# Performance work log

Hardware: AMD Instinct MI355X
Metric: run time of the kernel (lower is better)

Reference implementation:

```python
import jax, jax.numpy as jnp
import numpy as np

INPUT_WINDOW = 2048
HEAD_DIM = 128  # embedding_size // number_of_heads = 2048 // 16
TAU = 1.0
SCALE = 1.0 / ((INPUT_WINDOW * HEAD_DIM) ** 0.5 * TAU)


def setup_inputs() -> dict:
    key = jax.random.key(0)
    # (batch, number_of_series, length_input_window, hidden_dimensionality)
    x = jax.random.normal(key, (8, 16, 2048, 128), dtype=jnp.float32)
    return {"x": x}


def reference(x) -> jnp.ndarray:
    # Q = K = V = x; scores: [B, S, W, W]
    qk = jnp.einsum("bswd,bsud->bswu", x, x) * SCALE
    attn = jax.nn.softmax(qk, axis=-1)
    # dropout(p=0.1) is identity in eval mode
    out = jnp.einsum("bswu,bsud->bswd", attn, x)
    return out
```

## Files before the change

### kernel.cpp

```cpp
#include <hip/hip_runtime.h>
#include <hip/hip_bf16.h>


#define NSEQ   2048
#define DIM    128
#define KVBLK  64
#define EC (1.44269504088896f / 512.0f)

typedef short s8v __attribute__((ext_vector_type(8)));
typedef float f4   __attribute__((ext_vector_type(4)));
typedef float f16v __attribute__((ext_vector_type(16)));
typedef unsigned int u2 __attribute__((ext_vector_type(2)));
typedef unsigned int u4 __attribute__((ext_vector_type(4)));

__device__ __forceinline__ unsigned pk2(float a, float b) {
    union { __hip_bfloat162 h; unsigned u; } c;
    c.h = __float22bfloat162_rn(make_float2(a, b));
    return c.u;
}

__global__ __launch_bounds__(256, 2)
void attn_fwd(const float* __restrict__ x, float* __restrict__ out) {
    const int bid  = blockIdx.x;
    const int wg   = (bid & 7) * 256 + (bid >> 3);
    const int head = wg >> 4;
    const int qb   = wg & 15;

    const float* __restrict__ xh = x   + (size_t)head * (NSEQ * DIM);
    float* __restrict__       oh = out + (size_t)head * (NSEQ * DIM);

    const int tid  = threadIdx.x;
    const int lane = tid & 63;
    const int wave = tid >> 6;
    const int l31  = lane & 31;
    const int h    = lane >> 5;

    __shared__ __align__(16) short sK [KVBLK * DIM];
    __shared__ __align__(16) short sVt[DIM * KVBLK];

    const int qw0 = qb * 128 + wave * 32;
    s8v Qf[8];
    {
        const float* qp = xh + (size_t)(qw0 + l31) * DIM + 8 * h;
#pragma unroll
        for (int ks = 0; ks < 8; ++ks) {
            f4 a = *(const f4*)(qp + ks * 16);
            f4 b = *(const f4*)(qp + ks * 16 + 4);
            u4 q = { pk2(a[0], a[1]), pk2(a[2], a[3]), pk2(b[0], b[1]), pk2(b[2], b[3]) };
            Qf[ks] = *(s8v*)&q;
        }
    }

    f16v accO[4];
#pragma unroll
    for (int dt = 0; dt < 4; ++dt) accO[dt] = (f16v)(0.f);
    float lsum = 0.f;

    const int rw = tid >> 4;
    const int cg = tid & 15;

    f4 ld[8];
    {
        const float* s = xh + (size_t)(4 * rw) * DIM + 8 * cg;
#pragma unroll
        for (int i = 0; i < 4; ++i) {
            ld[2*i]   = *(const f4*)(s + i * DIM);
            ld[2*i+1] = *(const f4*)(s + i * DIM + 4);
        }
    }

    for (int kv0 = 0; kv0 < NSEQ; kv0 += KVBLK) {
#pragma unroll
        for (int i = 0; i < 4; ++i) {
            const int r  = 4 * rw + i;
            const int sz = ((r & 7) ^ ((r >> 3) & 7)) << 3;
            u4 kv = { pk2(ld[2*i][0],   ld[2*i][1]),   pk2(ld[2*i][2],   ld[2*i][3]),
                      pk2(ld[2*i+1][0], ld[2*i+1][1]), pk2(ld[2*i+1][2], ld[2*i+1][3]) };
            *(u4*)&sK[(r * DIM + 8 * cg) ^ sz] = kv;
        }
#pragma unroll
        for (int j = 0; j < 8; ++j) {
            const int d  = 8 * cg + j;
            const int sz = ((d & 7) ^ ((d >> 3) & 7)) << 3;
            const int hi = j >> 2, jj = j & 3;
            u2 vv = { pk2(ld[0 + hi][jj], ld[2 + hi][jj]),
                      pk2(ld[4 + hi][jj], ld[6 + hi][jj]) };
            *(u2*)&sVt[(d * KVBLK + 4 * rw) ^ sz] = vv;
        }
        __syncthreads();

        f16v accS[2];
        accS[0] = (f16v)(0.f); accS[1] = (f16v)(0.f);
        __builtin_amdgcn_s_setprio(1);
#pragma unroll
        for (int ut = 0; ut < 2; ++ut) {
            const int r    = ut * 32 + l31;
            const int sz   = ((r & 7) ^ ((r >> 3) & 7)) << 3;
            const int base = r * DIM + 8 * h;
#pragma unroll
            for (int ks = 0; ks < 8; ++ks) {
                s8v Kf = *(const s8v*)&sK[(base + ks * 16) ^ sz];
                accS[ut] = __builtin_amdgcn_mfma_f32_32x32x16_bf16(
                    Kf, Qf[ks], accS[ut], 0, 0, 0);
            }
        }
        __builtin_amdgcn_s_setprio(0);

        if (kv0 + KVBLK < NSEQ) {
            const float* s = xh + (size_t)(kv0 + KVBLK + 4 * rw) * DIM + 8 * cg;
#pragma unroll
            for (int i = 0; i < 4; ++i) {
                ld[2*i]   = *(const f4*)(s + i * DIM);
                ld[2*i+1] = *(const f4*)(s + i * DIM + 4);
            }
        }

        float part = 0.f;
#pragma unroll
        for (int ut = 0; ut < 2; ++ut)
#pragma unroll
            for (int r = 0; r < 16; ++r) {
                float v = exp2f(accS[ut][r] * EC);
                accS[ut][r] = v;
                part += v;
            }
        lsum += part;

        s8v Pf[4];
#pragma unroll
        for (int ks = 0; ks < 4; ++ks) {
#define PP(f) accS[(f) >> 4][(f) & 15]
            unsigned pa0 = pk2(PP(8*ks + 0), PP(8*ks + 1));
            unsigned pa1 = pk2(PP(8*ks + 2), PP(8*ks + 3));
            unsigned pb0 = pk2(PP(8*ks + 4), PP(8*ks + 5));
            unsigned pb1 = pk2(PP(8*ks + 6), PP(8*ks + 7));
#undef PP
            auto t0 = __builtin_amdgcn_permlane32_swap(pa0, pb0, false, false);
            auto t1 = __builtin_amdgcn_permlane32_swap(pa1, pb1, false, false);
            u4 w = { (unsigned)t0[0], (unsigned)t1[0], (unsigned)t0[1], (unsigned)t1[1] };
            Pf[ks] = *(s8v*)&w;
        }

        __builtin_amdgcn_s_setprio(1);
#pragma unroll
        for (int dt = 0; dt < 4; ++dt) {
            const int d    = dt * 32 + l31;
            const int sz   = ((d & 7) ^ ((d >> 3) & 7)) << 3;
            const int base = d * KVBLK + 8 * h;
#pragma unroll
            for (int ks = 0; ks < 4; ++ks) {
                s8v Vf = *(const s8v*)&sVt[(base + ks * 16) ^ sz];
                accO[dt] = __builtin_amdgcn_mfma_f32_32x32x16_bf16(
                    Pf[ks], Vf, accO[dt], 0, 0, 0);
            }
        }
        __builtin_amdgcn_s_setprio(0);
        __syncthreads();
    }

    const float tot = lsum + __shfl_xor(lsum, 32);
    const float inv = 1.f / tot;
#pragma unroll
    for (int r = 0; r < 16; ++r) {
        const int q       = (r & 3) + 8 * (r >> 2) + 4 * h;
        const float invq  = __shfl(inv, q, 32);
        float* op = oh + (size_t)(qw0 + q) * DIM + l31;
#pragma unroll
        for (int dt = 0; dt < 4; ++dt)
            op[dt * 32] = accO[dt][r] * invq;
    }
}

extern "C" void kernel_launch(void* const* d_in, const int* in_sizes, int n_in,
                              void* d_out, int out_size, void* d_ws, size_t ws_size,
                              hipStream_t stream) {
    const float* x = (const float*)d_in[0];
    float* out     = (float*)d_out;
    hipLaunchKernelGGL(attn_fwd, dim3(2048), dim3(256), 0, stream, x, out);
}
```

Measured before the change: 368.8 us.

## Pre-convert K/V to swizzled bf16 tiles and DMA them into double-buffered LDS

Adds a prepass kernel that converts each head's fp32 input into bf16 K and transposed V tiles already in the swizzled LDS layout, stored in the workspace. The attention kernel then streams these tiles with global_load_lds into double-buffered shared memory, overlapping the next tile's load with compute. This removes the repeated per-workgroup fp32 loads and bf16 conversion. It also folds the softmax scale into Q and uses the raw exp2 builtin. It costs an extra kernel launch, a large workspace with a fallback path, and doubled LDS usage.

```diff
diff --git a/kernel.cpp b/kernel.cpp
--- a/kernel.cpp
+++ b/kernel.cpp
@@ -5,6 +5,8 @@
 #define NSEQ   2048
 #define DIM    128
 #define KVBLK  64
+#define TILES  (NSEQ / KVBLK)
+#define IMG    (KVBLK * DIM)
 #define EC (1.44269504088896f / 512.0f)
 
 typedef short s8v __attribute__((ext_vector_type(8)));
@@ -13,14 +15,53 @@
 typedef unsigned int u2 __attribute__((ext_vector_type(2)));
 typedef unsigned int u4 __attribute__((ext_vector_type(4)));
 
+typedef __attribute__((address_space(1))) const void glob_t;
+typedef __attribute__((address_space(3))) void lds_t;
+
 __device__ __forceinline__ unsigned pk2(float a, float b) {
     union { __hip_bfloat162 h; unsigned u; } c;
     c.h = __float22bfloat162_rn(make_float2(a, b));
     return c.u;
 }
+__device__ __forceinline__ int swz(int r) { return ((r & 7) ^ ((r >> 3) & 7)) << 3; }
+
+__global__ __launch_bounds__(256)
+void prepass(const float* __restrict__ x, short* __restrict__ wsK,
+             short* __restrict__ wsV) {
+    const int b = blockIdx.x;
+    const float* src = x + (size_t)b * IMG;
+    short* dK = wsK + (size_t)b * IMG;
+    short* dV = wsV + (size_t)b * IMG;
+    const int rw = threadIdx.x >> 4;
+    const int cg = threadIdx.x & 15;
+
+    f4 ld[8];
+    const float* s = src + (size_t)(4 * rw) * DIM + 8 * cg;
+#pragma unroll
+    for (int i = 0; i < 4; ++i) {
+        ld[2*i]   = *(const f4*)(s + i * DIM);
+        ld[2*i+1] = *(const f4*)(s + i * DIM + 4);
+    }
+#pragma unroll
+    for (int i = 0; i < 4; ++i) {
+        const int r = 4 * rw + i;
+        u4 kv = { pk2(ld[2*i][0],   ld[2*i][1]),   pk2(ld[2*i][2],   ld[2*i][3]),
+                  pk2(ld[2*i+1][0], ld[2*i+1][1]), pk2(ld[2*i+1][2], ld[2*i+1][3]) };
+        *(u4*)&dK[(r * DIM + 8 * cg) ^ swz(r)] = kv;
+    }
+#pragma unroll
+    for (int j = 0; j < 8; ++j) {
+        const int d  = 8 * cg + j;
+        const int hi = j >> 2, jj = j & 3;
+        u2 vv = { pk2(ld[0 + hi][jj], ld[2 + hi][jj]),
+                  pk2(ld[4 + hi][jj], ld[6 + hi][jj]) };
+        *(u2*)&dV[(d * KVBLK + 4 * rw) ^ swz(d)] = vv;
+    }
+}
 
 __global__ __launch_bounds__(256, 2)
-void attn_fwd(const float* __restrict__ x, float* __restrict__ out) {
+void attn_lds(const float* __restrict__ x, const short* __restrict__ wsK,
+              const short* __restrict__ wsV, float* __restrict__ out) {
     const int bid  = blockIdx.x;
     const int wg   = (bid & 7) * 256 + (bid >> 3);
     const int head = wg >> 4;
@@ -28,6 +69,8 @@
 
     const float* __restrict__ xh = x   + (size_t)head * (NSEQ * DIM);
     float* __restrict__       oh = out + (size_t)head * (NSEQ * DIM);
+    const short* gK = wsK + (size_t)head * TILES * IMG;
+    const short* gV = wsV + (size_t)head * TILES * IMG;
 
     const int tid  = threadIdx.x;
     const int lane = tid & 63;
@@ -35,8 +78,8 @@
     const int l31  = lane & 31;
     const int h    = lane >> 5;
 
-    __shared__ __align__(16) short sK [KVBLK * DIM];
-    __shared__ __align__(16) short sVt[DIM * KVBLK];
+    __shared__ __align__(16) short sK [2][IMG];
+    __shared__ __align__(16) short sVt[2][IMG];
 
     const int qw0 = qb * 128 + wave * 32;
     s8v Qf[8];
@@ -46,7 +89,8 @@
         for (int ks = 0; ks < 8; ++ks) {
             f4 a = *(const f4*)(qp + ks * 16);
             f4 b = *(const f4*)(qp + ks * 16 + 4);
-            u4 q = { pk2(a[0], a[1]), pk2(a[2], a[3]), pk2(b[0], b[1]), pk2(b[2], b[3]) };
+            u4 q = { pk2(a[0] * EC, a[1] * EC), pk2(a[2] * EC, a[3] * EC),
+                     pk2(b[0] * EC, b[1] * EC), pk2(b[2] * EC, b[3] * EC) };
             Qf[ks] = *(s8v*)&q;
         }
     }
@@ -56,38 +100,25 @@
     for (int dt = 0; dt < 4; ++dt) accO[dt] = (f16v)(0.f);
     float lsum = 0.f;
 
-    const int rw = tid >> 4;
-    const int cg = tid & 15;
-
-    f4 ld[8];
-    {
-        const float* s = xh + (size_t)(4 * rw) * DIM + 8 * cg;
+    const int so = wave * 512 + lane * 8;
+    auto stage = [&](int b, int t) {
+        const short* srcK = gK + (size_t)t * IMG + so;
+        const short* srcV = gV + (size_t)t * IMG + so;
 #pragma unroll
         for (int i = 0; i < 4; ++i) {
-            ld[2*i]   = *(const f4*)(s + i * DIM);
-            ld[2*i+1] = *(const f4*)(s + i * DIM + 4);
-        }
-    }
-
-    for (int kv0 = 0; kv0 < NSEQ; kv0 += KVBLK) {
-#pragma unroll
-        for (int i = 0; i < 4; ++i) {
-            const int r  = 4 * rw + i;
-            const int sz = ((r & 7) ^ ((r >> 3) & 7)) << 3;
-            u4 kv = { pk2(ld[2*i][0],   ld[2*i][1]),   pk2(ld[2*i][2],   ld[2*i][3]),
-                      pk2(ld[2*i+1][0], ld[2*i+1][1]), pk2(ld[2*i+1][2], ld[2*i+1][3]) };
-            *(u4*)&sK[(r * DIM + 8 * cg) ^ sz] = kv;
-        }
-#pragma unroll
-        for (int j = 0; j < 8; ++j) {
-            const int d  = 8 * cg + j;
-            const int sz = ((d & 7) ^ ((d >> 3) & 7)) << 3;
-            const int hi = j >> 2, jj = j & 3;
-            u2 vv = { pk2(ld[0 + hi][jj], ld[2 + hi][jj]),
-                      pk2(ld[4 + hi][jj], ld[6 + hi][jj]) };
-            *(u2*)&sVt[(d * KVBLK + 4 * rw) ^ sz] = vv;
-        }
-        __syncthreads();
+            __builtin_amdgcn_global_load_lds((glob_t*)(srcK + i * 2048),
+                (lds_t*)&sK[b][wave * 512 + i * 2048], 16, 0, 0);
+            __builtin_amdgcn_global_load_lds((glob_t*)(srcV + i * 2048),
+                (lds_t*)&sVt[b][wave * 512 + i * 2048], 16, 0, 0);
+        }
+    };
+
+    stage(0, 0);
+    __syncthreads();
+    int buf = 0;
+
+    for (int t = 0; t < TILES; ++t) {
+        if (t + 1 < TILES) stage(buf ^ 1, t + 1);
 
         f16v accS[2];
         accS[0] = (f16v)(0.f); accS[1] = (f16v)(0.f);
@@ -95,32 +126,23 @@
 #pragma unroll
         for (int ut = 0; ut < 2; ++ut) {
             const int r    = ut * 32 + l31;
-            const int sz   = ((r & 7) ^ ((r >> 3) & 7)) << 3;
-            const int base = r * DIM + 8 * h;
+            const int base = (r * DIM + 8 * h);
+            const int sz   = swz(r);
 #pragma unroll
             for (int ks = 0; ks < 8; ++ks) {
-                s8v Kf = *(const s8v*)&sK[(base + ks * 16) ^ sz];
+                s8v Kf = *(const s8v*)&sK[buf][(base + ks * 16) ^ sz];
                 accS[ut] = __builtin_amdgcn_mfma_f32_32x32x16_bf16(
                     Kf, Qf[ks], accS[ut], 0, 0, 0);
             }
         }
         __builtin_amdgcn_s_setprio(0);
 
-        if (kv0 + KVBLK < NSEQ) {
-            const float* s = xh + (size_t)(kv0 + KVBLK + 4 * rw) * DIM + 8 * cg;
-#pragma unroll
-            for (int i = 0; i < 4; ++i) {
-                ld[2*i]   = *(const f4*)(s + i * DIM);
-                ld[2*i+1] = *(const f4*)(s + i * DIM + 4);
-            }
-        }
-
         float part = 0.f;
 #pragma unroll
         for (int ut = 0; ut < 2; ++ut)
 #pragma unroll
             for (int r = 0; r < 16; ++r) {
-                float v = exp2f(accS[ut][r] * EC);
+                float v = __builtin_amdgcn_exp2f(accS[ut][r]);
                 accS[ut][r] = v;
                 part += v;
             }
@@ -145,8 +167,148 @@
 #pragma unroll
         for (int dt = 0; dt < 4; ++dt) {
             const int d    = dt * 32 + l31;
-            const int sz   = ((d & 7) ^ ((d >> 3) & 7)) << 3;
             const int base = d * KVBLK + 8 * h;
+            const int sz   = swz(d);
+#pragma unroll
+            for (int ks = 0; ks < 4; ++ks) {
+                s8v Vf = *(const s8v*)&sVt[buf][(base + ks * 16) ^ sz];
+                accO[dt] = __builtin_amdgcn_mfma_f32_32x32x16_bf16(
+                    Pf[ks], Vf, accO[dt], 0, 0, 0);
+            }
+        }
+        __builtin_amdgcn_s_setprio(0);
+
+        __syncthreads();
+        buf ^= 1;
+    }
+
+    const float tot = lsum + __shfl_xor(lsum, 32);
+    const float inv = 1.f / tot;
+#pragma unroll
+    for (int r = 0; r < 16; ++r) {
+        const int q      = (r & 3) + 8 * (r >> 2) + 4 * h;
+        const float invq = __shfl(inv, q, 32);
+        float* op = oh + (size_t)(qw0 + q) * DIM + l31;
+#pragma unroll
+        for (int dt = 0; dt < 4; ++dt)
+            op[dt * 32] = accO[dt][r] * invq;
+    }
+}
+
+__global__ __launch_bounds__(256, 2)
+void attn_fwd_fb(const float* __restrict__ x, float* __restrict__ out) {
+    const int bid  = blockIdx.x;
+    const int wg   = (bid & 7) * 256 + (bid >> 3);
+    const int head = wg >> 4;
+    const int qb   = wg & 15;
+    const float* __restrict__ xh = x   + (size_t)head * (NSEQ * DIM);
+    float* __restrict__       oh = out + (size_t)head * (NSEQ * DIM);
+    const int tid  = threadIdx.x;
+    const int lane = tid & 63;
+    const int wave = tid >> 6;
+    const int l31  = lane & 31;
+    const int h    = lane >> 5;
+    __shared__ __align__(16) short sK [KVBLK * DIM];
+    __shared__ __align__(16) short sVt[DIM * KVBLK];
+    const int qw0 = qb * 128 + wave * 32;
+    s8v Qf[8];
+    {
+        const float* qp = xh + (size_t)(qw0 + l31) * DIM + 8 * h;
+#pragma unroll
+        for (int ks = 0; ks < 8; ++ks) {
+            f4 a = *(const f4*)(qp + ks * 16);
+            f4 b = *(const f4*)(qp + ks * 16 + 4);
+            u4 q = { pk2(a[0] * EC, a[1] * EC), pk2(a[2] * EC, a[3] * EC),
+                     pk2(b[0] * EC, b[1] * EC), pk2(b[2] * EC, b[3] * EC) };
+            Qf[ks] = *(s8v*)&q;
+        }
+    }
+    f16v accO[4];
+#pragma unroll
+    for (int dt = 0; dt < 4; ++dt) accO[dt] = (f16v)(0.f);
+    float lsum = 0.f;
+    const int rw = tid >> 4;
+    const int cg = tid & 15;
+    f4 ld[8];
+    {
+        const float* s = xh + (size_t)(4 * rw) * DIM + 8 * cg;
+#pragma unroll
+        for (int i = 0; i < 4; ++i) {
+            ld[2*i]   = *(const f4*)(s + i * DIM);
+            ld[2*i+1] = *(const f4*)(s + i * DIM + 4);
+        }
+    }
+    for (int kv0 = 0; kv0 < NSEQ; kv0 += KVBLK) {
+#pragma unroll
+        for (int i = 0; i < 4; ++i) {
+            const int r = 4 * rw + i;
+            u4 kv = { pk2(ld[2*i][0],   ld[2*i][1]),   pk2(ld[2*i][2],   ld[2*i][3]),
+                      pk2(ld[2*i+1][0], ld[2*i+1][1]), pk2(ld[2*i+1][2], ld[2*i+1][3]) };
+            *(u4*)&sK[(r * DIM + 8 * cg) ^ swz(r)] = kv;
+        }
+#pragma unroll
+        for (int j = 0; j < 8; ++j) {
+            const int d  = 8 * cg + j;
+            const int hi = j >> 2, jj = j & 3;
+            u2 vv = { pk2(ld[0 + hi][jj], ld[2 + hi][jj]),
+                      pk2(ld[4 + hi][jj], ld[6 + hi][jj]) };
+            *(u2*)&sVt[(d * KVBLK + 4 * rw) ^ swz(d)] = vv;
+        }
+        __syncthreads();
+        f16v accS[2];
+        accS[0] = (f16v)(0.f); accS[1] = (f16v)(0.f);
+        __builtin_amdgcn_s_setprio(1);
+#pragma unroll
+        for (int ut = 0; ut < 2; ++ut) {
+            const int r    = ut * 32 + l31;
+            const int base = r * DIM + 8 * h;
+            const int sz   = swz(r);
+#pragma unroll
+            for (int ks = 0; ks < 8; ++ks) {
+                s8v Kf = *(const s8v*)&sK[(base + ks * 16) ^ sz];
+                accS[ut] = __builtin_amdgcn_mfma_f32_32x32x16_bf16(
+                    Kf, Qf[ks], accS[ut], 0, 0, 0);
+            }
+        }
+        __builtin_amdgcn_s_setprio(0);
+        if (kv0 + KVBLK < NSEQ) {
+            const float* s = xh + (size_t)(kv0 + KVBLK + 4 * rw) * DIM + 8 * cg;
+#pragma unroll
+            for (int i = 0; i < 4; ++i) {
+                ld[2*i]   = *(const f4*)(s + i * DIM);
+                ld[2*i+1] = *(const f4*)(s + i * DIM + 4);
+            }
+        }
+        float part = 0.f;
+#pragma unroll
+        for (int ut = 0; ut < 2; ++ut)
+#pragma unroll
+            for (int r = 0; r < 16; ++r) {
+                float v = __builtin_amdgcn_exp2f(accS[ut][r]);
+                accS[ut][r] = v;
+                part += v;
+            }
+        lsum += part;
+        s8v Pf[4];
+#pragma unroll
+        for (int ks = 0; ks < 4; ++ks) {
+#define PP(f) accS[(f) >> 4][(f) & 15]
+            unsigned pa0 = pk2(PP(8*ks + 0), PP(8*ks + 1));
+            unsigned pa1 = pk2(PP(8*ks + 2), PP(8*ks + 3));
+            unsigned pb0 = pk2(PP(8*ks + 4), PP(8*ks + 5));
+            unsigned pb1 = pk2(PP(8*ks + 6), PP(8*ks + 7));
+#undef PP
+            auto t0 = __builtin_amdgcn_permlane32_swap(pa0, pb0, false, false);
+            auto t1 = __builtin_amdgcn_permlane32_swap(pa1, pb1, false, false);
+            u4 w = { (unsigned)t0[0], (unsigned)t1[0], (unsigned)t0[1], (unsigned)t1[1] };
+            Pf[ks] = *(s8v*)&w;
+        }
+        __builtin_amdgcn_s_setprio(1);
+#pragma unroll
+        for (int dt = 0; dt < 4; ++dt) {
+            const int d    = dt * 32 + l31;
+            const int base = d * KVBLK + 8 * h;
+            const int sz   = swz(d);
 #pragma unroll
             for (int ks = 0; ks < 4; ++ks) {
                 s8v Vf = *(const s8v*)&sVt[(base + ks * 16) ^ sz];
@@ -157,13 +319,12 @@
         __builtin_amdgcn_s_setprio(0);
         __syncthreads();
     }
-
     const float tot = lsum + __shfl_xor(lsum, 32);
     const float inv = 1.f / tot;
 #pragma unroll
     for (int r = 0; r < 16; ++r) {
-        const int q       = (r & 3) + 8 * (r >> 2) + 4 * h;
-        const float invq  = __shfl(inv, q, 32);
+        const int q      = (r & 3) + 8 * (r >> 2) + 4 * h;
+        const float invq = __shfl(inv, q, 32);
         float* op = oh + (size_t)(qw0 + q) * DIM + l31;
 #pragma unroll
         for (int dt = 0; dt < 4; ++dt)
@@ -176,5 +337,13 @@
                               hipStream_t stream) {
     const float* x = (const float*)d_in[0];
     float* out     = (float*)d_out;
-    hipLaunchKernelGGL(attn_fwd, dim3(2048), dim3(256), 0, stream, x, out);
-}
+    const size_t need = (size_t)2 * 128 * TILES * IMG * sizeof(short);
+    if (ws_size >= need) {
+        short* wsK = (short*)d_ws;
+        short* wsV = wsK + (size_t)128 * TILES * IMG;
+        hipLaunchKernelGGL(prepass, dim3(128 * TILES), dim3(256), 0, stream, x, wsK, wsV);
+        hipLaunchKernelGGL(attn_lds, dim3(2048), dim3(256), 0, stream, x, wsK, wsV, out);
+    } else {
+        hipLaunchKernelGGL(attn_fwd_fb, dim3(2048), dim3(256), 0, stream, x, out);
+    }
+}
```

New measurement: 362.5 us. Within noise of the previous version (-1.7%).
